# Kernel optimization log

Measured on AMD Instinct MI355X. Metric: run time of the kernel, lower is better.

Reference implementation:

```python
import jax, jax.numpy as jnp
import numpy as np

B, SIZE, TRACK = 4096, 1024, 1024  # batch, input size, tracker_size


def setup_inputs() -> dict:
    key = jax.random.key(0)
    ks = jax.random.split(key, 9)
    s = 0.02  # small init scale to keep gates in a sane range
    return {
        "top_buf_h": jax.random.normal(ks[0], (B, SIZE), jnp.float32),
        "top_stack1_h": jax.random.normal(ks[1], (B, SIZE), jnp.float32),
        "top_stack2_h": jax.random.normal(ks[2], (B, SIZE), jnp.float32),
        "h_prev": jax.random.normal(ks[3], (B, TRACK), jnp.float32),
        "c_prev": jax.random.normal(ks[4], (B, TRACK), jnp.float32),
        "W_buf": jax.random.normal(ks[5], (SIZE, 4 * TRACK), jnp.float32) * s,
        "W_stack1": jax.random.normal(ks[6], (SIZE, 4 * TRACK), jnp.float32) * s,
        "W_stack2": jax.random.normal(ks[7], (SIZE, 4 * TRACK), jnp.float32) * s,
        "W_lateral": jax.random.normal(ks[8], (TRACK, 4 * TRACK), jnp.float32) * s,
        "b_lateral": jnp.zeros((4 * TRACK,), jnp.float32),
    }


def reference(top_buf_h, top_stack1_h, top_stack2_h, h_prev, c_prev,
              W_buf, W_stack1, W_stack2, W_lateral, b_lateral):
    # Fused tracker step: 3 bias-free projections + lateral projection (with bias)
    gates = (top_buf_h @ W_buf
             + top_stack1_h @ W_stack1
             + top_stack2_h @ W_stack2
             + h_prev @ W_lateral
             + b_lateral)                      # [B, 4*TRACK]
    # SPINN lstm(c_prev, gates): chunk order (a, i, f, o)
    a, i, f, o = jnp.split(gates, 4, axis=1)
    c = jnp.tanh(a) * jax.nn.sigmoid(i) + jax.nn.sigmoid(f) * c_prev
    h = jax.nn.sigmoid(o) * jnp.tanh(c)
    return (h, c)
```

## Files before the change

kernel.cpp:

```cpp
#include <hip/hip_runtime.h>


typedef __bf16 bf16x8 __attribute__((ext_vector_type(8)));
typedef float  f32x4  __attribute__((ext_vector_type(4)));

__device__ __forceinline__ unsigned short f2bf(float x) {
    unsigned int u = __builtin_bit_cast(unsigned int, x);
    u = (u + 0x7fffu + ((u >> 16) & 1u)) >> 16;
    return (unsigned short)u;
}

__device__ __forceinline__ void gl2lds16(const unsigned short* g, unsigned short* l) {
    __builtin_amdgcn_global_load_lds(
        (const __attribute__((address_space(1))) unsigned int*)g,
        (__attribute__((address_space(3))) unsigned int*)l,
        16, 0, 0);
}

__device__ __forceinline__ float sigf(float x) {
    return __builtin_amdgcn_rcpf(1.f + __expf(-x));
}
__device__ __forceinline__ float tanh_fast(float x) {
    return 2.f * __builtin_amdgcn_rcpf(1.f + __expf(-2.f * x)) - 1.f;
}


__global__ void convert_A(const float* __restrict__ A0, const float* __restrict__ A1,
                          const float* __restrict__ A2, const float* __restrict__ A3,
                          unsigned short* __restrict__ Abf) {
    int idx = blockIdx.x * 256 + threadIdx.x;
    int e0  = idx * 4;
    int b   = e0 >> 12;
    int k   = e0 & 4095;
    const float* S = (k < 1024) ? A0 : (k < 2048) ? A1 : (k < 3072) ? A2 : A3;
    int col = k & 1023;
    const float4 v = *reinterpret_cast<const float4*>(S + (size_t)b * 1024 + col);
    ushort4 o;
    o.x = f2bf(v.x); o.y = f2bf(v.y); o.z = f2bf(v.z); o.w = f2bf(v.w);
    *reinterpret_cast<ushort4*>(Abf + (size_t)b * 4096 + k) = o;
}


__global__ void convert_B(const float* __restrict__ Wb, const float* __restrict__ W1,
                          const float* __restrict__ W2, const float* __restrict__ Wl,
                          unsigned short* __restrict__ Bt) {
    __shared__ float t[32][33];
    int tile = blockIdx.x;
    int jt = tile & 127, kt = tile >> 7;
    int j0 = jt * 32, k0 = kt * 32;
    int ksel = k0 >> 10;
    const float* S = (ksel == 0) ? Wb : (ksel == 1) ? W1 : (ksel == 2) ? W2 : Wl;
    int kloc = k0 & 1023;
    int tx = threadIdx.x & 31, ty = threadIdx.x >> 5;
#pragma unroll
    for (int i = 0; i < 4; ++i) {
        int r = ty + i * 8;
        t[r][tx] = S[(size_t)(kloc + r) * 4096 + j0 + tx];
    }
    __syncthreads();
    int g = j0 >> 10;
    int nbase = j0 & 1023;
#pragma unroll
    for (int i = 0; i < 4; ++i) {
        int jj = ty + i * 8;
        int u  = nbase + jj;
        int p  = (u >> 6) * 256 + ((u >> 4) & 3) * 64 + g * 16 + (u & 15);
        Bt[(size_t)p * 4096 + k0 + tx] = f2bf(t[tx][jj]);
    }
}


__global__ __launch_bounds__(512, 2) void gemm_lstm(
        const unsigned short* __restrict__ A,
        const unsigned short* __restrict__ Bt,
        const float* __restrict__ bias,
        const float* __restrict__ cprev,
        float* __restrict__ out) {
    __shared__ unsigned short lds[65536];
#define ASB(b) (lds + (b) * 16384)
#define BSB(b) (lds + 32768 + (b) * 16384)

    const int tid  = threadIdx.x;
    const int wid  = tid >> 6;
    const int lane = tid & 63;
    const int wm = wid >> 2, wn = wid & 3;
    const int lr = lane & 15, lq = lane >> 4;
    const int bm = blockIdx.y, bc = blockIdx.x;

    const int X0 = wid * 1024 + lane * 16;
    const int rs = X0 >> 7;
    const int cs = ((X0 & 127) ^ ((rs & 7) << 4)) >> 1;
    const unsigned short* Agb = A  + ((size_t)(bm * 256 + rs)) * 4096 + cs;
    const unsigned short* Bgb = Bt + ((size_t)(bc * 256 + rs)) * 4096 + cs;

    const int swz = (lr & 7) << 4;
    const int ca0 = ((lq * 16) ^ swz) >> 1;
    const int ca1 = ((64 + lq * 16) ^ swz) >> 1;

    f32x4 acc[8][4] = {};

#define STAGE_A(b, h, kt) do {                                               \
        unsigned short* _d = ASB(b) + (h) * 8192 + wid * 512;                \
        const unsigned short* _s = Agb + (size_t)((h) * 128) * 4096 + (kt) * 64; \
        gl2lds16(_s, _d);                                                    \
        gl2lds16(_s + 64 * 4096, _d + 4096);                                 \
    } while (0)
#define STAGE_B(b, h, kt) do {                                               \
        unsigned short* _d = BSB(b) + (h) * 8192 + wid * 512;                \
        const unsigned short* _s = Bgb + (size_t)((h) * 128) * 4096 + (kt) * 64; \
        gl2lds16(_s, _d);                                                    \
        gl2lds16(_s + 64 * 4096, _d + 4096);                                 \
    } while (0)
#define LDA(buf, mi, cax) (*reinterpret_cast<const bf16x8*>((buf) + (wm * 128 + (mi) * 16 + lr) * 64 + (cax)))
#define LDB(buf, ni, cax) (*reinterpret_cast<const bf16x8*>((buf) + (wn * 64  + (ni) * 16 + lr) * 64 + (cax)))
#define BARRIER() asm volatile("s_barrier" ::: "memory")
#define MFMA16(P)                                                            \
        __builtin_amdgcn_s_setprio(1);                                       \
        _Pragma("unroll")                                                    \
        for (int m = 0; m < 2; ++m)                                          \
        _Pragma("unroll")                                                    \
        for (int ks = 0; ks < 2; ++ks)                                       \
        _Pragma("unroll")                                                    \
        for (int ni = 0; ni < 4; ++ni)                                       \
            acc[(P)*2 + m][ni] = __builtin_amdgcn_mfma_f32_16x16x32_bf16(    \
                af[m][ks], bfr[ni][ks], acc[(P)*2 + m][ni], 0, 0, 0);        \
        __builtin_amdgcn_s_setprio(0)

    STAGE_A(0, 0, 0); STAGE_A(0, 1, 0);
    STAGE_B(0, 0, 0); STAGE_B(0, 1, 0);
    STAGE_B(1, 0, 1); STAGE_B(1, 1, 1);
    asm volatile("s_waitcnt vmcnt(4)" ::: "memory");
    BARRIER();

    for (int t = 0; t < 64; ++t) {
        const unsigned short* Ac = ASB(t & 1);
        const unsigned short* Bc = BSB(t & 1);
        const int bn  = (t & 1) ^ 1;
        const int bb  = t & 1;
        const int ktA = (t < 63) ? t + 1 : 63;
        const int ktB = (t < 62) ? t + 2 : 63;

        bf16x8 bfr[4][2];
        {
            bf16x8 af[2][2];
#pragma unroll
            for (int ni = 0; ni < 4; ++ni) { bfr[ni][0] = LDB(Bc, ni, ca0); bfr[ni][1] = LDB(Bc, ni, ca1); }
#pragma unroll
            for (int m = 0; m < 2; ++m) { af[m][0] = LDA(Ac, 0 + m, ca0); af[m][1] = LDA(Ac, 0 + m, ca1); }
            STAGE_A(bn, 0, ktA);
            BARRIER();
            MFMA16(0);
            BARRIER();
        }
        {
            bf16x8 af[2][2];
#pragma unroll
            for (int m = 0; m < 2; ++m) { af[m][0] = LDA(Ac, 2 + m, ca0); af[m][1] = LDA(Ac, 2 + m, ca1); }
            STAGE_A(bn, 1, ktA);
            BARRIER();
            MFMA16(1);
            BARRIER();
        }
        {
            bf16x8 af[2][2];
#pragma unroll
            for (int m = 0; m < 2; ++m) { af[m][0] = LDA(Ac, 4 + m, ca0); af[m][1] = LDA(Ac, 4 + m, ca1); }
            STAGE_B(bb, 0, ktB);
            BARRIER();
            MFMA16(2);
            BARRIER();
        }
        {
            bf16x8 af[2][2];
#pragma unroll
            for (int m = 0; m < 2; ++m) { af[m][0] = LDA(Ac, 6 + m, ca0); af[m][1] = LDA(Ac, 6 + m, ca1); }
            STAGE_B(bb, 1, ktB);
            BARRIER();
            MFMA16(3);
            asm volatile("s_waitcnt vmcnt(4)" ::: "memory");
            BARRIER();
        }
    }

    const int u = bc * 64 + wn * 16 + lr;
    const float ba  = bias[u];
    const float bi  = bias[1024 + u];
    const float bfv = bias[2048 + u];
    const float bo  = bias[3072 + u];
    float* outh = out;
    float* outc = out + (size_t)4096 * 1024;

#pragma unroll
    for (int mi = 0; mi < 8; ++mi) {
        const int r0 = bm * 256 + wm * 128 + mi * 16 + lq * 4;
#pragma unroll
        for (int r = 0; r < 4; ++r) {
            const size_t off = (size_t)(r0 + r) * 1024 + u;
            const float a  = acc[mi][0][r] + ba;
            const float ii = acc[mi][1][r] + bi;
            const float ff = acc[mi][2][r] + bfv;
            const float oo = acc[mi][3][r] + bo;
            const float c  = tanh_fast(a) * sigf(ii) + sigf(ff) * cprev[off];
            outh[off] = sigf(oo) * tanh_fast(c);
            outc[off] = c;
        }
    }
#undef STAGE_A
#undef STAGE_B
#undef LDA
#undef LDB
#undef BARRIER
#undef MFMA16
#undef ASB
#undef BSB
}


extern "C" void kernel_launch(void* const* d_in, const int* in_sizes, int n_in,
                              void* d_out, int out_size, void* d_ws, size_t ws_size,
                              hipStream_t stream) {
    const float* top_buf = (const float*)d_in[0];
    const float* s1      = (const float*)d_in[1];
    const float* s2      = (const float*)d_in[2];
    const float* hprev   = (const float*)d_in[3];
    const float* cprev   = (const float*)d_in[4];
    const float* Wb      = (const float*)d_in[5];
    const float* W1      = (const float*)d_in[6];
    const float* W2      = (const float*)d_in[7];
    const float* Wl      = (const float*)d_in[8];
    const float* bl      = (const float*)d_in[9];

    unsigned short* Abf = (unsigned short*)d_ws;
    unsigned short* Bt  = Abf + (size_t)4096 * 4096;

    convert_A<<<16384, 256, 0, stream>>>(top_buf, s1, s2, hprev, Abf);
    convert_B<<<16384, 256, 0, stream>>>(Wb, W1, W2, Wl, Bt);

    dim3 grid(16, 16);
    gemm_lstm<<<grid, 512, 0, stream>>>(Abf, Bt, bl, cprev, (float*)d_out);
}
```

Baseline: 151.2 us.

## Merge conversion kernels into one launch and relax GEMM barrier scheduling

Fuses the two fp32-to-bf16 conversion kernels into a single launch that branches on block index, removing one kernel launch and its tail. In the GEMM main loop, the inline-asm barriers with memory clobbers become the builtin barrier plus an explicit lgkmcnt(0) wait before the MFMAs, and the K loop is unrolled by two. This aims to give the compiler more freedom to schedule LDS reads and to cut launch overhead. The explicit wait may serialize LDS latency, and unrolling raises register pressure.

```diff
diff --git a/kernel.cpp b/kernel.cpp
--- a/kernel.cpp
+++ b/kernel.cpp
@@ -25,47 +25,47 @@
 }
 
 
-__global__ void convert_A(const float* __restrict__ A0, const float* __restrict__ A1,
-                          const float* __restrict__ A2, const float* __restrict__ A3,
-                          unsigned short* __restrict__ Abf) {
-    int idx = blockIdx.x * 256 + threadIdx.x;
-    int e0  = idx * 4;
-    int b   = e0 >> 12;
-    int k   = e0 & 4095;
-    const float* S = (k < 1024) ? A0 : (k < 2048) ? A1 : (k < 3072) ? A2 : A3;
-    int col = k & 1023;
-    const float4 v = *reinterpret_cast<const float4*>(S + (size_t)b * 1024 + col);
-    ushort4 o;
-    o.x = f2bf(v.x); o.y = f2bf(v.y); o.z = f2bf(v.z); o.w = f2bf(v.w);
-    *reinterpret_cast<ushort4*>(Abf + (size_t)b * 4096 + k) = o;
-}
-
-
-__global__ void convert_B(const float* __restrict__ Wb, const float* __restrict__ W1,
-                          const float* __restrict__ W2, const float* __restrict__ Wl,
-                          unsigned short* __restrict__ Bt) {
+__global__ void convert_AB(const float* __restrict__ A0, const float* __restrict__ A1,
+                           const float* __restrict__ A2, const float* __restrict__ A3,
+                           const float* __restrict__ Wb, const float* __restrict__ W1,
+                           const float* __restrict__ W2, const float* __restrict__ Wl,
+                           unsigned short* __restrict__ Abf,
+                           unsigned short* __restrict__ Bt) {
     __shared__ float t[32][33];
-    int tile = blockIdx.x;
-    int jt = tile & 127, kt = tile >> 7;
-    int j0 = jt * 32, k0 = kt * 32;
-    int ksel = k0 >> 10;
-    const float* S = (ksel == 0) ? Wb : (ksel == 1) ? W1 : (ksel == 2) ? W2 : Wl;
-    int kloc = k0 & 1023;
-    int tx = threadIdx.x & 31, ty = threadIdx.x >> 5;
-#pragma unroll
-    for (int i = 0; i < 4; ++i) {
-        int r = ty + i * 8;
-        t[r][tx] = S[(size_t)(kloc + r) * 4096 + j0 + tx];
-    }
-    __syncthreads();
-    int g = j0 >> 10;
-    int nbase = j0 & 1023;
-#pragma unroll
-    for (int i = 0; i < 4; ++i) {
-        int jj = ty + i * 8;
-        int u  = nbase + jj;
-        int p  = (u >> 6) * 256 + ((u >> 4) & 3) * 64 + g * 16 + (u & 15);
-        Bt[(size_t)p * 4096 + k0 + tx] = f2bf(t[tx][jj]);
+    if (blockIdx.x < 16384) {
+        int idx = blockIdx.x * 256 + threadIdx.x;
+        int e0  = idx * 4;
+        int b   = e0 >> 12;
+        int k   = e0 & 4095;
+        const float* S = (k < 1024) ? A0 : (k < 2048) ? A1 : (k < 3072) ? A2 : A3;
+        int col = k & 1023;
+        const float4 v = *reinterpret_cast<const float4*>(S + (size_t)b * 1024 + col);
+        ushort4 o;
+        o.x = f2bf(v.x); o.y = f2bf(v.y); o.z = f2bf(v.z); o.w = f2bf(v.w);
+        *reinterpret_cast<ushort4*>(Abf + (size_t)b * 4096 + k) = o;
+    } else {
+        int tile = blockIdx.x - 16384;
+        int jt = tile & 127, kt = tile >> 7;
+        int j0 = jt * 32, k0 = kt * 32;
+        int ksel = k0 >> 10;
+        const float* S = (ksel == 0) ? Wb : (ksel == 1) ? W1 : (ksel == 2) ? W2 : Wl;
+        int kloc = k0 & 1023;
+        int tx = threadIdx.x & 31, ty = threadIdx.x >> 5;
+#pragma unroll
+        for (int i = 0; i < 4; ++i) {
+            int r = ty + i * 8;
+            t[r][tx] = S[(size_t)(kloc + r) * 4096 + j0 + tx];
+        }
+        __syncthreads();
+        int g = j0 >> 10;
+        int nbase = j0 & 1023;
+#pragma unroll
+        for (int i = 0; i < 4; ++i) {
+            int jj = ty + i * 8;
+            int u  = nbase + jj;
+            int p  = (u >> 6) * 256 + ((u >> 4) & 3) * 64 + g * 16 + (u & 15);
+            Bt[(size_t)p * 4096 + k0 + tx] = f2bf(t[tx][jj]);
+        }
     }
 }
 
@@ -113,7 +113,8 @@
     } while (0)
 #define LDA(buf, mi, cax) (*reinterpret_cast<const bf16x8*>((buf) + (wm * 128 + (mi) * 16 + lr) * 64 + (cax)))
 #define LDB(buf, ni, cax) (*reinterpret_cast<const bf16x8*>((buf) + (wn * 64  + (ni) * 16 + lr) * 64 + (cax)))
-#define BARRIER() asm volatile("s_barrier" ::: "memory")
+#define SBAR() __builtin_amdgcn_s_barrier()
+#define LGK0() asm volatile("s_waitcnt lgkmcnt(0)")
 #define MFMA16(P)                                                            \
         __builtin_amdgcn_s_setprio(1);                                       \
         _Pragma("unroll")                                                    \
@@ -130,8 +131,9 @@
     STAGE_B(0, 0, 0); STAGE_B(0, 1, 0);
     STAGE_B(1, 0, 1); STAGE_B(1, 1, 1);
     asm volatile("s_waitcnt vmcnt(4)" ::: "memory");
-    BARRIER();
-
+    SBAR();
+
+#pragma unroll 2
     for (int t = 0; t < 64; ++t) {
         const unsigned short* Ac = ASB(t & 1);
         const unsigned short* Bc = BSB(t & 1);
@@ -148,37 +150,41 @@
 #pragma unroll
             for (int m = 0; m < 2; ++m) { af[m][0] = LDA(Ac, 0 + m, ca0); af[m][1] = LDA(Ac, 0 + m, ca1); }
             STAGE_A(bn, 0, ktA);
-            BARRIER();
+            SBAR();
+            LGK0();
             MFMA16(0);
-            BARRIER();
+            SBAR();
         }
         {
             bf16x8 af[2][2];
 #pragma unroll
             for (int m = 0; m < 2; ++m) { af[m][0] = LDA(Ac, 2 + m, ca0); af[m][1] = LDA(Ac, 2 + m, ca1); }
             STAGE_A(bn, 1, ktA);
-            BARRIER();
+            SBAR();
+            LGK0();
             MFMA16(1);
-            BARRIER();
+            SBAR();
         }
         {
             bf16x8 af[2][2];
 #pragma unroll
             for (int m = 0; m < 2; ++m) { af[m][0] = LDA(Ac, 4 + m, ca0); af[m][1] = LDA(Ac, 4 + m, ca1); }
             STAGE_B(bb, 0, ktB);
-            BARRIER();
+            SBAR();
+            LGK0();
             MFMA16(2);
-            BARRIER();
+            SBAR();
         }
         {
             bf16x8 af[2][2];
 #pragma unroll
             for (int m = 0; m < 2; ++m) { af[m][0] = LDA(Ac, 6 + m, ca0); af[m][1] = LDA(Ac, 6 + m, ca1); }
             STAGE_B(bb, 1, ktB);
-            BARRIER();
+            SBAR();
+            LGK0();
             MFMA16(3);
             asm volatile("s_waitcnt vmcnt(4)" ::: "memory");
-            BARRIER();
+            SBAR();
         }
     }
 
@@ -209,7 +215,8 @@
 #undef STAGE_B
 #undef LDA
 #undef LDB
-#undef BARRIER
+#undef SBAR
+#undef LGK0
 #undef MFMA16
 #undef ASB
 #undef BSB
@@ -233,8 +240,8 @@
     unsigned short* Abf = (unsigned short*)d_ws;
     unsigned short* Bt  = Abf + (size_t)4096 * 4096;
 
-    convert_A<<<16384, 256, 0, stream>>>(top_buf, s1, s2, hprev, Abf);
-    convert_B<<<16384, 256, 0, stream>>>(Wb, W1, W2, Wl, Bt);
+    convert_AB<<<32768, 256, 0, stream>>>(top_buf, s1, s2, hprev,
+                                          Wb, W1, W2, Wl, Abf, Bt);
 
     dim3 grid(16, 16);
     gemm_lstm<<<grid, 512, 0, stream>>>(Abf, Bt, bl, cprev, (float*)d_out);
```

After: 147.1 us. 1.03x faster.
